# Performance work log

Hardware: AMD Instinct MI355X
Metric: run time of the kernel (lower is better)

Reference implementation:

```python
import jax, jax.numpy as jnp
import numpy as np

DIM = 512
HEADS = 16
WIN = (7, 7)
S = WIN[0] * WIN[1]          # 49 tokens per window
NW = 64                      # windows per image (mask dim)
B_IMG = 32
B = B_IMG * NW               # 2048 total windows
TABLE = (2 * WIN[0] - 1) * (2 * WIN[1] - 1)  # 169


def _relative_position_index():
    ch = np.arange(WIN[0]); cw = np.arange(WIN[1])
    coords = np.stack(np.meshgrid(ch, cw, indexing='ij')).reshape(2, -1)  # [2, S]
    rel = coords[:, :, None] - coords[:, None, :]                          # [2, S, S]
    rel = rel.transpose(1, 2, 0).astype(np.int32)
    rel[:, :, 0] += WIN[0] - 1
    rel[:, :, 1] += WIN[1] - 1
    rel[:, :, 0] *= 2 * WIN[1] - 1
    return rel.sum(-1)  # [S, S], values in [0, TABLE)


def setup_inputs() -> dict:
    key = jax.random.key(0)
    ks = jax.random.split(key, 7)
    return {
        'x': jax.random.normal(ks[0], (B, S, DIM), jnp.float32),
        'mask': jax.random.normal(ks[1], (NW, S, S), jnp.float32),
        'qkv_w': jax.random.normal(ks[2], (DIM, 3 * DIM), jnp.float32) * (DIM ** -0.5),
        'qkv_b': jax.random.normal(ks[3], (3 * DIM,), jnp.float32) * 0.02,
        'proj_w': jax.random.normal(ks[4], (DIM, DIM), jnp.float32) * (DIM ** -0.5),
        'proj_b': jax.random.normal(ks[5], (DIM,), jnp.float32) * 0.02,
        'bias_table': jax.random.normal(ks[6], (TABLE, HEADS), jnp.float32) * 0.02,
        'rel_idx': jnp.asarray(_relative_position_index()),
    }


def reference(x, mask, qkv_w, qkv_b, proj_w, proj_b, bias_table, rel_idx):
    b, s, c = x.shape
    hd = c // HEADS
    scale = hd ** -0.5
    qkv = x @ qkv_w + qkv_b                                   # [B, S, 3C]
    qkv = qkv.reshape(b, s, 3, HEADS, hd).transpose(2, 0, 3, 1, 4)
    q, k, v = qkv[0], qkv[1], qkv[2]                          # [B, H, S, hd]
    attn = jnp.einsum('bhqd,bhkd->bhqk', q * scale, k)        # [B, H, S, S]
    # gathered relative position bias: [S*S, H] -> [H, S, S]
    bias = bias_table[rel_idx.reshape(-1)].reshape(s, s, HEADS).transpose(2, 0, 1)
    attn = attn + bias[None]
    # shifted-window mask add
    nw = mask.shape[0]
    attn = attn.reshape(-1, nw, HEADS, s, s) + mask[None, :, None]
    attn = attn.reshape(-1, HEADS, s, s)
    attn = jax.nn.softmax(attn, axis=-1)
    out = jnp.einsum('bhqk,bhkd->bhqd', attn, v)              # [B, H, S, hd]
    out = out.transpose(0, 2, 1, 3).reshape(b, s, c)
    return out @ proj_w + proj_b
```

## Files before the change

### kernel.cpp

```cpp
#include <hip/hip_runtime.h>


typedef unsigned short u16;
typedef __attribute__((ext_vector_type(8))) short short8;
typedef __attribute__((ext_vector_type(4))) float floatx4;

#define B_WIN 2048
#define SEQ 49
#define DIM 512
#define NHEAD 16
#define HD 32
#define MROWS (B_WIN * SEQ)
#define QTOT 51380224u
#define VOFF 102760448u

__device__ __forceinline__ u16 f2bf(float x) {
    unsigned u = __float_as_uint(x);
    u += 0x7fffu + ((u >> 16) & 1u);
    return (u16)(u >> 16);
}

__device__ __forceinline__ void async_ld16(const void* g, void* l) {
    __builtin_amdgcn_global_load_lds(
        (const __attribute__((address_space(1))) void*)g,
        (__attribute__((address_space(3))) void*)l, 16, 0, 0);
}

__global__ void conv_f32_bf16(const float* __restrict__ in, u16* __restrict__ out, int n4) {
    int id = blockIdx.x * 256 + threadIdx.x;
    if (id >= n4) return;
    float4 v = ((const float4*)in)[id];
    uint2 o;
    o.x = (unsigned)f2bf(v.x) | ((unsigned)f2bf(v.y) << 16);
    o.y = (unsigned)f2bf(v.z) | ((unsigned)f2bf(v.w) << 16);
    *(uint2*)(out + (size_t)id * 4) = o;
}

__global__ void transpose_conv(const float* __restrict__ in, u16* __restrict__ out, int Cn) {
    int id = blockIdx.x * 256 + threadIdx.x;
    if (id >= Cn * 512) return;
    int k = id & 511;
    int n = id >> 9;
    out[id] = f2bf(in[(size_t)k * Cn + n]);
}

__global__ void build_combined(const float* __restrict__ mask, const float* __restrict__ bias_table,
                               const int* __restrict__ rel_idx, float* __restrict__ cmb) {
    int id = blockIdx.x * 256 + threadIdx.x;
    if (id >= 64 * 16 * 49 * 64) return;
    int w64 = id & 63;
    int j   = w64 & 3;
    int l   = w64 >> 2;
    int c   = j * 16 + l;
    int t   = id >> 6;
    int row = t % 49;
    int wh  = t / 49;
    int h = wh & 15, w = wh >> 4;
    float v = -1.0e30f;
    if (c < 49) {
        int ij = row * 49 + c;
        v = bias_table[rel_idx[ij] * NHEAD + h] + mask[(size_t)w * 2401 + ij];
    }
    cmb[id] = v;
}

__global__ void zero_vpad(u16* __restrict__ qkvp) {
    int id = blockIdx.x * 256 + threadIdx.x;
    if (id >= 2048 * 16 * 32) return;
    uint4 z = {0u, 0u, 0u, 0u};
    u16* p = qkvp + VOFF + (size_t)id * 64 + 48;
    *(uint4*)p = z;
    *((uint4*)p + 1) = z;
}

__global__ __launch_bounds__(256, 2)
void gemm_qkv(const u16* __restrict__ A, const u16* __restrict__ Bt,
              const float* __restrict__ bias, u16* __restrict__ qkvp) {
    const int K = 512;
    const int tid  = threadIdx.x;
    const int lane = tid & 63, wave = tid >> 6;
    const int quad = lane >> 4, l16 = lane & 15;
    const int wr = wave >> 1, wc = wave & 1;

    const int flat = blockIdx.y * 12 + blockIdx.x;
    const int swz  = (flat & 7) * 1176 + (flat >> 3);
    const int bx = swz % 12;
    const int by = swz / 12;
    const int m0 = by * 128, n0 = bx * 128;

    __shared__ u16 smem[128 * 136];
    u16* As = smem;
    u16* Bs = smem + 4096;

    const int f0 = (wave * 2 + 0) * 512 + lane * 8;
    const int f1 = (wave * 2 + 1) * 512 + lane * 8;
    const int r0 = f0 >> 5, c0 = f0 & 31;
    const int r1 = f1 >> 5, c1 = f1 & 31;
    const u16* Ab = A + (size_t)m0 * K;
    const u16* Bb = Bt + (size_t)n0 * K;

    floatx4 acc[4][4] = {};

    for (int kt = 0; kt < K; kt += 32) {
        async_ld16(Ab + (size_t)r0 * K + kt + c0, &As[f0]);
        async_ld16(Ab + (size_t)r1 * K + kt + c1, &As[f1]);
        async_ld16(Bb + (size_t)r0 * K + kt + c0, &Bs[f0]);
        async_ld16(Bb + (size_t)r1 * K + kt + c1, &Bs[f1]);
        __syncthreads();
        short8 af[4], bf[4];
#pragma unroll
        for (int i = 0; i < 4; ++i)
            af[i] = *(const short8*)&As[(wr * 64 + i * 16 + l16) * 32 + quad * 8];
#pragma unroll
        for (int j = 0; j < 4; ++j)
            bf[j] = *(const short8*)&Bs[(wc * 64 + j * 16 + l16) * 32 + quad * 8];
#pragma unroll
        for (int i = 0; i < 4; ++i)
#pragma unroll
            for (int j = 0; j < 4; ++j)
                acc[i][j] = __builtin_amdgcn_mfma_f32_16x16x32_bf16(af[i], bf[j], acc[i][j], 0, 0, 0);
        __syncthreads();
    }

#pragma unroll
    for (int j = 0; j < 4; ++j) {
        const int col = wc * 64 + j * 16 + l16;
        const float bv = bias[n0 + col];
#pragma unroll
        for (int i = 0; i < 4; ++i)
#pragma unroll
            for (int r = 0; r < 4; ++r) {
                const int row = wr * 64 + i * 16 + quad * 4 + r;
                smem[row * 136 + col] = f2bf(acc[i][j][r] + bv);
            }
    }
    __syncthreads();

    if (n0 < 1024) {
        const int c   = n0 >> 9;
        const int hh0 = (n0 & 511) >> 5;
        u16* base = qkvp + (size_t)c * QTOT;
#pragma unroll
        for (int it = 0; it < 8; ++it) {
            const int idx  = it * 256 + tid;
            const int row  = idx >> 4;
            const int hb   = (idx >> 2) & 3;
            const int part = idx & 3;
            short8 v = *(const short8*)&smem[row * 136 + hb * 32 + part * 8];
            const int rg = m0 + row;
            const int b2 = (int)((unsigned)rg / 49u);
            const int s  = rg - b2 * 49;
            *(short8*)(base + (size_t)(b2 * 16 + hh0 + hb) * 1568 + s * 32 + part * 8) = v;
        }
    } else {
        const int hh0 = (n0 - 1024) >> 5;
        u16* base = qkvp + VOFF;
#pragma unroll 16
        for (int it = 0; it < 64; ++it) {
            const int idx = it * 256 + tid;
            const int col = idx >> 7;
            const int row = idx & 127;
            const u16 v = smem[row * 136 + col];
            const int rg = m0 + row;
            const int b2 = (int)((unsigned)rg / 49u);
            const int s  = rg - b2 * 49;
            const int hh = hh0 + (col >> 5);
            const int d  = col & 31;
            base[(size_t)(b2 * 16 + hh) * 2048 + d * 64 + s] = v;
        }
    }
}

__global__ __launch_bounds__(256, 2)
void gemm_bt(const u16* __restrict__ A, const u16* __restrict__ Bt,
             const float* __restrict__ bias, float* __restrict__ Cout,
             int M, int N, int K) {
    const int tid  = threadIdx.x;
    const int lane = tid & 63, wave = tid >> 6;
    const int quad = lane >> 4, l16 = lane & 15;
    const int wr = wave >> 1, wc = wave & 1;

    const int nbx = gridDim.x, nby = gridDim.y;
    const int total = nbx * nby;
    const int flat = blockIdx.y * nbx + blockIdx.x;
    const int swz = ((total & 7) == 0) ? ((flat & 7) * (total >> 3) + (flat >> 3)) : flat;
    const int bx = swz % nbx;
    const int by = swz / nbx;
    const int m0 = by * 128, n0 = bx * 128;

    __shared__ u16 As[128 * 32];
    __shared__ u16 Bs[128 * 32];

    const int f0 = (wave * 2 + 0) * 512 + lane * 8;
    const int f1 = (wave * 2 + 1) * 512 + lane * 8;
    const int r0 = f0 >> 5, c0 = f0 & 31;
    const int r1 = f1 >> 5, c1 = f1 & 31;
    const u16* Ab = A + (size_t)m0 * K;
    const u16* Bb = Bt + (size_t)n0 * K;

    floatx4 acc[4][4] = {};

    for (int kt = 0; kt < K; kt += 32) {
        async_ld16(Ab + (size_t)r0 * K + kt + c0, &As[f0]);
        async_ld16(Ab + (size_t)r1 * K + kt + c1, &As[f1]);
        async_ld16(Bb + (size_t)r0 * K + kt + c0, &Bs[f0]);
        async_ld16(Bb + (size_t)r1 * K + kt + c1, &Bs[f1]);
        __syncthreads();
        short8 af[4], bf[4];
#pragma unroll
        for (int i = 0; i < 4; ++i)
            af[i] = *(const short8*)&As[(wr * 64 + i * 16 + l16) * 32 + quad * 8];
#pragma unroll
        for (int j = 0; j < 4; ++j)
            bf[j] = *(const short8*)&Bs[(wc * 64 + j * 16 + l16) * 32 + quad * 8];
#pragma unroll
        for (int i = 0; i < 4; ++i)
#pragma unroll
            for (int j = 0; j < 4; ++j)
                acc[i][j] = __builtin_amdgcn_mfma_f32_16x16x32_bf16(af[i], bf[j], acc[i][j], 0, 0, 0);
        __syncthreads();
    }

#pragma unroll
    for (int i = 0; i < 4; ++i) {
#pragma unroll
        for (int j = 0; j < 4; ++j) {
            int col = n0 + wc * 64 + j * 16 + l16;
            float bv = bias[col];
#pragma unroll
            for (int r = 0; r < 4; ++r) {
                int row = m0 + wr * 64 + i * 16 + quad * 4 + r;
                Cout[(size_t)row * N + col] = acc[i][j][r] + bv;
            }
        }
    }
}

__global__ __launch_bounds__(64, 4)
void attn2(const u16* __restrict__ qkvp, const float* __restrict__ cmbp,
           u16* __restrict__ out) {
    const int lane = threadIdx.x;
    const int quad = lane >> 4, l16 = lane & 15;
    const int p0 = blockIdx.x * 2;
    const int b  = p0 >> 4, h0 = p0 & 15;

    const u16* qb0 = qkvp + (size_t)p0 * 1568;
    const u16* kb0 = qb0 + QTOT;
    const u16* qb1 = qb0 + 1568;
    const u16* kb1 = kb0 + 1568;
    const u16* vb0 = qkvp + VOFF + (size_t)p0 * 2048;
    const u16* vb1 = vb0 + 2048;

    const float* cb0 = cmbp + (size_t)(((b & 63) * 16 + h0) * 49) * 64;
    const float* cb1 = cb0 + 49 * 64;

    u16* op0 = out + (size_t)b * SEQ * DIM + h0 * HD;
    u16* op1 = op0 + HD;

    __shared__ u16 ps[64 * 72];

    int rr[4];
#pragma unroll
    for (int i = 0; i < 4; ++i) { int r = i * 16 + l16; rr[i] = r > 48 ? 48 : r; }

    short8 af0[4], bf0[4], af1[4], bf1[4];
#pragma unroll
    for (int i = 0; i < 4; ++i) af0[i] = *(const short8*)(qb0 + rr[i] * 32 + quad * 8);
#pragma unroll
    for (int j = 0; j < 4; ++j) bf0[j] = *(const short8*)(kb0 + rr[j] * 32 + quad * 8);
#pragma unroll
    for (int i = 0; i < 4; ++i) af1[i] = *(const short8*)(qb1 + rr[i] * 32 + quad * 8);
#pragma unroll
    for (int j = 0; j < 4; ++j) bf1[j] = *(const short8*)(kb1 + rr[j] * 32 + quad * 8);

    const float scale = 0.1767766952966369f;

    auto do_pair = [&](const short8* af, const short8* bfr, const float* cb,
                       const u16* vb, u16* op) {
        short8 vf[2][2];
#pragma unroll
        for (int kt = 0; kt < 2; ++kt)
#pragma unroll
            for (int jn = 0; jn < 2; ++jn)
                vf[kt][jn] = *(const short8*)(vb + (jn * 16 + l16) * 64 + kt * 32 + quad * 8);

#pragma unroll
        for (int i = 0; i < 4; ++i) {
            floatx4 accS[4] = {};
#pragma unroll
            for (int j = 0; j < 4; ++j)
                accS[j] = __builtin_amdgcn_mfma_f32_16x16x32_bf16(af[i], bfr[j], accS[j], 0, 0, 0);
            const int rbase = i * 16 + quad * 4;
#pragma unroll
            for (int r = 0; r < 4; ++r) {
                const int row = rbase + r;
                const int rc = row < 48 ? row : 48;
                float4 c4 = *(const float4*)(cb + rc * 64 + l16 * 4);
                float x[4] = { accS[0][r] * scale + c4.x, accS[1][r] * scale + c4.y,
                               accS[2][r] * scale + c4.z, accS[3][r] * scale + c4.w };
                float m = fmaxf(fmaxf(x[0], x[1]), fmaxf(x[2], x[3]));
#pragma unroll
                for (int off = 1; off < 16; off <<= 1) m = fmaxf(m, __shfl_xor(m, off));
                float e[4], s = 0.f;
#pragma unroll
                for (int j = 0; j < 4; ++j) { e[j] = __expf(x[j] - m); s += e[j]; }
#pragma unroll
                for (int off = 1; off < 16; off <<= 1) s += __shfl_xor(s, off);
                float inv = __builtin_amdgcn_rcpf(s);
#pragma unroll
                for (int j = 0; j < 4; ++j)
                    ps[row * 72 + j * 16 + l16] = f2bf(e[j] * inv);
            }
        }
        __syncthreads();

        floatx4 accO[4][2] = {};
#pragma unroll
        for (int kt = 0; kt < 2; ++kt) {
            short8 pf[4];
#pragma unroll
            for (int i = 0; i < 4; ++i)
                pf[i] = *(const short8*)&ps[(i * 16 + l16) * 72 + kt * 32 + quad * 8];
#pragma unroll
            for (int i = 0; i < 4; ++i)
#pragma unroll
                for (int jn = 0; jn < 2; ++jn)
                    accO[i][jn] = __builtin_amdgcn_mfma_f32_16x16x32_bf16(pf[i], vf[kt][jn], accO[i][jn], 0, 0, 0);
        }
        __syncthreads();

#pragma unroll
        for (int i = 0; i < 4; ++i)
#pragma unroll
            for (int jn = 0; jn < 2; ++jn)
#pragma unroll
                for (int r = 0; r < 4; ++r) {
                    int row = i * 16 + quad * 4 + r;
                    if (row < SEQ)
                        op[(size_t)row * DIM + jn * 16 + l16] = f2bf(accO[i][jn][r]);
                }
    };

    do_pair(af0, bf0, cb0, vb0, op0);
    do_pair(af1, bf1, cb1, vb1, op1);
}

extern "C" void kernel_launch(void* const* d_in, const int* in_sizes, int n_in,
                              void* d_out, int out_size, void* d_ws, size_t ws_size,
                              hipStream_t stream) {
    const float* x         = (const float*)d_in[0];
    const float* mask      = (const float*)d_in[1];
    const float* qkv_w     = (const float*)d_in[2];
    const float* qkv_b     = (const float*)d_in[3];
    const float* proj_w    = (const float*)d_in[4];
    const float* proj_b    = (const float*)d_in[5];
    const float* bias_tab  = (const float*)d_in[6];
    const int*   rel_idx   = (const int*)d_in[7];
    float* out = (float*)d_out;

    char* ws = (char*)d_ws;
    u16*   xbf     = (u16*)(ws + 0);
    u16*   qkvp    = (u16*)(ws + 102760448);
    u16*   wqkv_t  = (u16*)(ws + 452333568);
    u16*   wproj_t = (u16*)(ws + 453906432);
    float* cmb     = out;

    conv_f32_bf16<<<50176, 256, 0, stream>>>(x, xbf, 12845056);
    transpose_conv<<<3072, 256, 0, stream>>>(qkv_w, wqkv_t, 1536);
    transpose_conv<<<1024, 256, 0, stream>>>(proj_w, wproj_t, 512);
    build_combined<<<12544, 256, 0, stream>>>(mask, bias_tab, rel_idx, cmb);
    zero_vpad<<<4096, 256, 0, stream>>>(qkvp);
    gemm_qkv<<<dim3(12, 784), 256, 0, stream>>>(xbf, wqkv_t, qkv_b, qkvp);
    attn2<<<B_WIN * NHEAD / 2, 64, 0, stream>>>(qkvp, cmb, xbf);
    gemm_bt<<<dim3(4, 784), 256, 0, stream>>>(xbf, wproj_t, proj_b, out,
                                              MROWS, 512, 512);
}
```

Measured before the change: 856.2 us.

## Split QKV GEMM into Q/K and V launches, use exp2 softmax with deferred normalization

The QKV GEMM is split into two templated launches, one writing the Q/K layout and one the padded V layout. This removes the runtime branch and lets each launch use its own tile swizzle. Softmax now folds log2(e) into the scale and the combined bias/mask so it can use the native exp2 instead of __expf. Normalization is deferred: unnormalized probabilities are stored to LDS as bf16 and the output is multiplied by the reciprocal after the PV MFMA. This saves per-element multiplies but stores unnormalized values in bf16, which slightly changes rounding.

```diff
diff --git a/kernel.cpp b/kernel.cpp
--- a/kernel.cpp
+++ b/kernel.cpp
@@ -46,6 +46,7 @@
 
 __global__ void build_combined(const float* __restrict__ mask, const float* __restrict__ bias_table,
                                const int* __restrict__ rel_idx, float* __restrict__ cmb) {
+    const float LOG2E = 1.4426950408889634f;
     int id = blockIdx.x * 256 + threadIdx.x;
     if (id >= 64 * 16 * 49 * 64) return;
     int w64 = id & 63;
@@ -59,7 +60,7 @@
     float v = -1.0e30f;
     if (c < 49) {
         int ij = row * 49 + c;
-        v = bias_table[rel_idx[ij] * NHEAD + h] + mask[(size_t)w * 2401 + ij];
+        v = (bias_table[rel_idx[ij] * NHEAD + h] + mask[(size_t)w * 2401 + ij]) * LOG2E;
     }
     cmb[id] = v;
 }
@@ -73,20 +74,21 @@
     *((uint4*)p + 1) = z;
 }
 
+template<int NBX, int NB8, int NBASE, bool ISV>
 __global__ __launch_bounds__(256, 2)
-void gemm_qkv(const u16* __restrict__ A, const u16* __restrict__ Bt,
-              const float* __restrict__ bias, u16* __restrict__ qkvp) {
+void gemm_qkv_part(const u16* __restrict__ A, const u16* __restrict__ Bt,
+                   const float* __restrict__ bias, u16* __restrict__ qkvp) {
     const int K = 512;
     const int tid  = threadIdx.x;
     const int lane = tid & 63, wave = tid >> 6;
     const int quad = lane >> 4, l16 = lane & 15;
     const int wr = wave >> 1, wc = wave & 1;
 
-    const int flat = blockIdx.y * 12 + blockIdx.x;
-    const int swz  = (flat & 7) * 1176 + (flat >> 3);
-    const int bx = swz % 12;
-    const int by = swz / 12;
-    const int m0 = by * 128, n0 = bx * 128;
+    const int flat = blockIdx.y * NBX + blockIdx.x;
+    const int swz  = (flat & 7) * NB8 + (flat >> 3);
+    const int bx = swz % NBX;
+    const int by = swz / NBX;
+    const int m0 = by * 128, n0 = NBASE + bx * 128;
 
     __shared__ u16 smem[128 * 136];
     u16* As = smem;
@@ -136,7 +138,7 @@
     }
     __syncthreads();
 
-    if (n0 < 1024) {
+    if constexpr (!ISV) {
         const int c   = n0 >> 9;
         const int hh0 = (n0 & 511) >> 5;
         u16* base = qkvp + (size_t)c * QTOT;
@@ -273,7 +275,7 @@
 #pragma unroll
     for (int j = 0; j < 4; ++j) bf1[j] = *(const short8*)(kb1 + rr[j] * 32 + quad * 8);
 
-    const float scale = 0.1767766952966369f;
+    const float scale2 = 0.2550348754f;
 
     auto do_pair = [&](const short8* af, const short8* bfr, const float* cb,
                        const u16* vb, u16* op) {
@@ -283,6 +285,8 @@
 #pragma unroll
             for (int jn = 0; jn < 2; ++jn)
                 vf[kt][jn] = *(const short8*)(vb + (jn * 16 + l16) * 64 + kt * 32 + quad * 8);
+
+        float sinv[4][4];
 
 #pragma unroll
         for (int i = 0; i < 4; ++i) {
@@ -296,20 +300,20 @@
                 const int row = rbase + r;
                 const int rc = row < 48 ? row : 48;
                 float4 c4 = *(const float4*)(cb + rc * 64 + l16 * 4);
-                float x[4] = { accS[0][r] * scale + c4.x, accS[1][r] * scale + c4.y,
-                               accS[2][r] * scale + c4.z, accS[3][r] * scale + c4.w };
+                float x[4] = { accS[0][r] * scale2 + c4.x, accS[1][r] * scale2 + c4.y,
+                               accS[2][r] * scale2 + c4.z, accS[3][r] * scale2 + c4.w };
                 float m = fmaxf(fmaxf(x[0], x[1]), fmaxf(x[2], x[3]));
 #pragma unroll
                 for (int off = 1; off < 16; off <<= 1) m = fmaxf(m, __shfl_xor(m, off));
                 float e[4], s = 0.f;
 #pragma unroll
-                for (int j = 0; j < 4; ++j) { e[j] = __expf(x[j] - m); s += e[j]; }
+                for (int j = 0; j < 4; ++j) { e[j] = __builtin_amdgcn_exp2f(x[j] - m); s += e[j]; }
 #pragma unroll
                 for (int off = 1; off < 16; off <<= 1) s += __shfl_xor(s, off);
-                float inv = __builtin_amdgcn_rcpf(s);
+                sinv[i][r] = __builtin_amdgcn_rcpf(s);
 #pragma unroll
                 for (int j = 0; j < 4; ++j)
-                    ps[row * 72 + j * 16 + l16] = f2bf(e[j] * inv);
+                    ps[row * 72 + j * 16 + l16] = f2bf(e[j]);
             }
         }
         __syncthreads();
@@ -332,13 +336,15 @@
 #pragma unroll
         for (int i = 0; i < 4; ++i)
 #pragma unroll
-            for (int jn = 0; jn < 2; ++jn)
-#pragma unroll
-                for (int r = 0; r < 4; ++r) {
-                    int row = i * 16 + quad * 4 + r;
-                    if (row < SEQ)
-                        op[(size_t)row * DIM + jn * 16 + l16] = f2bf(accO[i][jn][r]);
+            for (int r = 0; r < 4; ++r) {
+                const int row = i * 16 + quad * 4 + r;
+                if (row < SEQ) {
+                    const float inv = sinv[i][r];
+#pragma unroll
+                    for (int jn = 0; jn < 2; ++jn)
+                        op[(size_t)row * DIM + jn * 16 + l16] = f2bf(accO[i][jn][r] * inv);
                 }
+            }
     };
 
     do_pair(af0, bf0, cb0, vb0, op0);
@@ -370,7 +376,8 @@
     transpose_conv<<<1024, 256, 0, stream>>>(proj_w, wproj_t, 512);
     build_combined<<<12544, 256, 0, stream>>>(mask, bias_tab, rel_idx, cmb);
     zero_vpad<<<4096, 256, 0, stream>>>(qkvp);
-    gemm_qkv<<<dim3(12, 784), 256, 0, stream>>>(xbf, wqkv_t, qkv_b, qkvp);
+    gemm_qkv_part<8, 784, 0,    false><<<dim3(8, 784), 256, 0, stream>>>(xbf, wqkv_t, qkv_b, qkvp);
+    gemm_qkv_part<4, 392, 1024, true ><<<dim3(4, 784), 256, 0, stream>>>(xbf, wqkv_t, qkv_b, qkvp);
     attn2<<<B_WIN * NHEAD / 2, 64, 0, stream>>>(qkvp, cmb, xbf);
     gemm_bt<<<dim3(4, 784), 256, 0, stream>>>(xbf, wproj_t, proj_b, out,
                                               MROWS, 512, 512);
```

After: 911.3 us. 1.06x slower.
